# Kernel optimization log

Measured on AMD Instinct MI355X. Metric: run time of the kernel, lower is better.

Reference implementation:

```python
import jax, jax.numpy as jnp
import numpy as np

L, V, Tctx, D, H, DFF = 4, 32000, 1024, 1024, 16, 4096
HD = D // H
B, T = 2, 1024


def _ln(x, w, b):
    mu = jnp.mean(x, axis=-1, keepdims=True)
    var = jnp.var(x, axis=-1, keepdims=True)
    return (x - mu) * jax.lax.rsqrt(var + 1e-5) * w + b


def setup_inputs() -> dict:
    key = jax.random.key(0)
    ks = jax.random.split(key, 8)
    s = 0.02
    return {
        "idx": jax.random.randint(ks[0], (B, T), 0, V),
        "wte": jax.random.normal(ks[1], (V, D), jnp.float32) * s,
        "wpe": jax.random.normal(ks[2], (Tctx, D), jnp.float32) * s,
        "ln1_w": jnp.ones((L, D), jnp.float32),
        "ln1_b": jnp.zeros((L, D), jnp.float32),
        "qkv_w": jax.random.normal(ks[3], (L, 3 * D, D), jnp.float32) * s,
        "qkv_b": jnp.zeros((L, 3 * D), jnp.float32),
        "proj_w": jax.random.normal(ks[4], (L, D, D), jnp.float32) * s,
        "proj_b": jnp.zeros((L, D), jnp.float32),
        "ln2_w": jnp.ones((L, D), jnp.float32),
        "ln2_b": jnp.zeros((L, D), jnp.float32),
        "fc1_w": jax.random.normal(ks[5], (L, DFF, D), jnp.float32) * s,
        "fc1_b": jnp.zeros((L, DFF), jnp.float32),
        "fc2_w": jax.random.normal(ks[6], (L, D, DFF), jnp.float32) * s,
        "fc2_b": jnp.zeros((L, D), jnp.float32),
        "lnf_w": jnp.ones((D,), jnp.float32),
        "lnf_b": jnp.zeros((D,), jnp.float32),
    }


def reference(idx, wte, wpe, ln1_w, ln1_b, qkv_w, qkv_b, proj_w, proj_b,
              ln2_w, ln2_b, fc1_w, fc1_b, fc2_w, fc2_b, lnf_w, lnf_b):
    b, t = idx.shape
    x = wte[idx] + wpe[:t]  # (B,T,D); dropout=0 (eval)
    scale = 1.0 / jnp.sqrt(jnp.float32(HD))
    causal = jnp.tril(jnp.ones((t, t), bool))  # (T,T)

    def block(x, p):
        (l1w, l1b, qw, qb, pw, pb, l2w, l2b, f1w, f1b, f2w, f2b) = p
        h = _ln(x, l1w, l1b)
        qkv = h @ qw.T + qb  # (B,T,3D)
        q, k, v = jnp.split(qkv, 3, axis=-1)
        q = q.reshape(b, t, H, HD)
        k = k.reshape(b, t, H, HD)
        v = v.reshape(b, t, H, HD)
        att = jnp.einsum('bqhd,bkhd->bhqk', q, k) * scale
        att = jnp.where(causal, att, -jnp.inf)
        att = jax.nn.softmax(att, axis=-1)
        y = jnp.einsum('bhqk,bkhd->bqhd', att, v).reshape(b, t, D)
        x = x + y @ pw.T + pb
        h2 = _ln(x, l2w, l2b)
        h2 = jax.nn.gelu(h2 @ f1w.T + f1b, approximate=False)
        x = x + h2 @ f2w.T + f2b
        return x, None

    params = (ln1_w, ln1_b, qkv_w, qkv_b, proj_w, proj_b,
              ln2_w, ln2_b, fc1_w, fc1_b, fc2_w, fc2_b)
    x, _ = jax.lax.scan(block, x, params)
    x = _ln(x, lnf_w, lnf_b)
    logits = x @ wte.T  # weight-tied lm_head
    return logits
```

## Files before the change

kernel.cpp:

```cpp
#include <hip/hip_runtime.h>
#include <hip/hip_bf16.h>
#include <cstdint>
#include <cstddef>

using hb = __hip_bfloat16;
typedef __bf16 bf16x8 __attribute__((ext_vector_type(8)));
typedef float f32x4 __attribute__((ext_vector_type(4)));
typedef const __attribute__((address_space(1))) void* gptr_t;
typedef __attribute__((address_space(3))) void* lptr_t;

namespace {
constexpr int L_ = 4, V_ = 32000, D_ = 1024, H_ = 16, DFF_ = 4096, HD_ = 64;
constexpr int B_ = 2, T_ = 1024;
constexpr int BT = B_ * T_;
constexpr int PSTR = 56;
constexpr int MTILES = BT / 128;
}

__global__ __launch_bounds__(256) void k_cast_bf16(const float* __restrict__ in,
                                                   hb* __restrict__ out, int n4) {
  int i = blockIdx.x * 256 + threadIdx.x;
  const int stride = gridDim.x * 256;
  for (; i < n4; i += stride) {
    float4 v = reinterpret_cast<const float4*>(in)[i];
    union { hb h[4]; ushort4 u; } t;
    t.h[0] = __float2bfloat16(v.x);
    t.h[1] = __float2bfloat16(v.y);
    t.h[2] = __float2bfloat16(v.z);
    t.h[3] = __float2bfloat16(v.w);
    reinterpret_cast<ushort4*>(out)[i] = t.u;
  }
}

__global__ __launch_bounds__(256) void k_embed(const int* __restrict__ idx,
                                               const float* __restrict__ wte,
                                               const float* __restrict__ wpe,
                                               float* __restrict__ x) {
  const int i = blockIdx.x * 256 + threadIdx.x;
  const int row = i >> 10;
  const int d = i & 1023;
  const int t = row & (T_ - 1);
  const int tok = idx[row];
  x[i] = wte[(size_t)tok * D_ + d] + wpe[(size_t)t * D_ + d];
}

__global__ __launch_bounds__(256) void k_ln(const float* __restrict__ x,
                                            const float* __restrict__ w,
                                            const float* __restrict__ b,
                                            hb* __restrict__ out) {
  const int row = blockIdx.x;
  const int tid = threadIdx.x;
  const float4 v = reinterpret_cast<const float4*>(x + (size_t)row * D_)[tid];
  float s = v.x + v.y + v.z + v.w;
  float ss = v.x * v.x + v.y * v.y + v.z * v.z + v.w * v.w;
#pragma unroll
  for (int o = 32; o; o >>= 1) { s += __shfl_xor(s, o); ss += __shfl_xor(ss, o); }
  __shared__ float rs[4], rss[4];
  const int wid = tid >> 6;
  if ((tid & 63) == 0) { rs[wid] = s; rss[wid] = ss; }
  __syncthreads();
  s = rs[0] + rs[1] + rs[2] + rs[3];
  ss = rss[0] + rss[1] + rss[2] + rss[3];
  const float mu = s * (1.f / D_);
  const float var = ss * (1.f / D_) - mu * mu;
  const float rstd = rsqrtf(var + 1e-5f);
  const float4 wv = reinterpret_cast<const float4*>(w)[tid];
  const float4 bv = reinterpret_cast<const float4*>(b)[tid];
  union { hb h[4]; ushort4 u; } t;
  t.h[0] = __float2bfloat16((v.x - mu) * rstd * wv.x + bv.x);
  t.h[1] = __float2bfloat16((v.y - mu) * rstd * wv.y + bv.y);
  t.h[2] = __float2bfloat16((v.z - mu) * rstd * wv.z + bv.z);
  t.h[3] = __float2bfloat16((v.w - mu) * rstd * wv.w + bv.w);
  reinterpret_cast<ushort4*>(out + (size_t)row * D_)[tid] = t.u;
}

__global__ __launch_bounds__(256) void k_vtrans(const hb* __restrict__ qkv,
                                                hb* __restrict__ vt) {
  __shared__ __align__(16) hb tile[64][66];
  const int bh = blockIdx.x;
  const int b = bh >> 4, h = bh & (H_ - 1);
  const int t0 = blockIdx.y * 64;
  const int tid = threadIdx.x;
  const int tl = tid >> 2, dc = (tid & 3) * 16;
  const hb* src = qkv + ((size_t)(b * T_ + t0 + tl) * 3 * D_) + 2 * D_ + h * HD_ + dc;
  *reinterpret_cast<bf16x8*>(&tile[tl][dc]) = *reinterpret_cast<const bf16x8*>(src);
  *reinterpret_cast<bf16x8*>(&tile[tl][dc + 8]) = *reinterpret_cast<const bf16x8*>(src + 8);
  __syncthreads();
  const int d = tid & 63, tj = tid >> 6;
  hb o[16];
#pragma unroll
  for (int j = 0; j < 16; ++j) o[j] = tile[tj * 16 + j][d];
  bf16x8* dst = reinterpret_cast<bf16x8*>(vt + ((size_t)bh * HD_ + d) * T_ + t0 + tj * 16);
  dst[0] = *reinterpret_cast<bf16x8*>(&o[0]);
  dst[1] = *reinterpret_cast<bf16x8*>(&o[8]);
}

__global__ __launch_bounds__(256) void k_attn(const hb* __restrict__ qkv,
                                              const hb* __restrict__ vt,
                                              hb* __restrict__ y) {
  const int lane = threadIdx.x & 63;
  const int wid = threadIdx.x >> 6;
  const int gw = blockIdx.x * 4 + wid;
  const int qt = 63 - (gw & 63);
  const int bh = gw >> 6;
  const int h = bh & (H_ - 1), b = bh >> 4;
  const int q0 = qt * 16;
  const int lr = lane & 15, g = lane >> 4;

  __shared__ __align__(16) hb plds[4][16 * PSTR];
  hb* pw = plds[wid];

  const size_t qrow = ((size_t)(b * T_ + q0 + lr) * 3 * D_) + (size_t)h * HD_;
  const bf16x8 qa0 = *reinterpret_cast<const bf16x8*>(qkv + qrow + g * 8);
  const bf16x8 qa1 = *reinterpret_cast<const bf16x8*>(qkv + qrow + 32 + g * 8);

  const f32x4 z = {0.f, 0.f, 0.f, 0.f};
  float m[4] = {-1e30f, -1e30f, -1e30f, -1e30f};
  float lsum[4] = {0.f, 0.f, 0.f, 0.f};
  f32x4 o[4];
#pragma unroll
  for (int i = 0; i < 4; ++i) o[i] = z;

  const int nkv = (q0 + 47) >> 5;
  for (int kt = 0; kt < nkv; ++kt) {
    const int kv0 = kt * 32;
    f32x4 s[2];
#pragma unroll
    for (int nt = 0; nt < 2; ++nt) {
      const size_t krow =
          ((size_t)(b * T_ + kv0 + nt * 16 + lr) * 3 * D_) + D_ + (size_t)h * HD_;
      const bf16x8 kb0 = *reinterpret_cast<const bf16x8*>(qkv + krow + g * 8);
      const bf16x8 kb1 = *reinterpret_cast<const bf16x8*>(qkv + krow + 32 + g * 8);
      f32x4 acc = z;
      acc = __builtin_amdgcn_mfma_f32_16x16x32_bf16(qa0, kb0, acc, 0, 0, 0);
      acc = __builtin_amdgcn_mfma_f32_16x16x32_bf16(qa1, kb1, acc, 0, 0, 0);
      s[nt] = acc;
    }
#pragma unroll
    for (int r = 0; r < 4; ++r) {
      const int qg = q0 + g * 4 + r;
      const float s0 = (kv0 + lr <= qg) ? s[0][r] * 0.125f : -1e30f;
      const float s1 = (kv0 + 16 + lr <= qg) ? s[1][r] * 0.125f : -1e30f;
      float rmax = fmaxf(s0, s1);
#pragma unroll
      for (int off = 1; off < 16; off <<= 1) rmax = fmaxf(rmax, __shfl_xor(rmax, off));
      const float mn = fmaxf(m[r], rmax);
      const float c = __expf(m[r] - mn);
      m[r] = mn;
      const float p0 = __expf(s0 - mn);
      const float p1 = __expf(s1 - mn);
      float ps = p0 + p1;
#pragma unroll
      for (int off = 1; off < 16; off <<= 1) ps += __shfl_xor(ps, off);
      lsum[r] = lsum[r] * c + ps;
#pragma unroll
      for (int dt = 0; dt < 4; ++dt) o[dt][r] *= c;
      pw[(g * 4 + r) * PSTR + lr] = __float2bfloat16(p0);
      pw[(g * 4 + r) * PSTR + 16 + lr] = __float2bfloat16(p1);
    }
    const bf16x8 pa = *reinterpret_cast<const bf16x8*>(&pw[lr * PSTR + g * 8]);
#pragma unroll
    for (int dt = 0; dt < 4; ++dt) {
      const bf16x8 vb = *reinterpret_cast<const bf16x8*>(
          vt + ((size_t)bh * HD_ + dt * 16 + lr) * T_ + kv0 + g * 8);
      o[dt] = __builtin_amdgcn_mfma_f32_16x16x32_bf16(pa, vb, o[dt], 0, 0, 0);
    }
  }
#pragma unroll
  for (int dt = 0; dt < 4; ++dt) {
#pragma unroll
    for (int r = 0; r < 4; ++r) {
      const size_t oo =
          ((size_t)(b * T_ + q0 + g * 4 + r) * D_) + h * HD_ + dt * 16 + lr;
      y[oo] = __float2bfloat16(o[dt][r] / lsum[r]);
    }
  }
}

template <int EPI, bool OBF, int BN>
__global__ __launch_bounds__(256) void gemm_bt(const hb* __restrict__ A,
                                               const hb* __restrict__ Bw,
                                               const float* __restrict__ bias,
                                               const float* resid,
                                               void* outv, int M, int N, int K) {
  constexpr int WMR = (BN == 128) ? 4 : 2;
  __shared__ __align__(16) hb As[2][128 * 32];
  __shared__ __align__(16) hb Bs[2][BN * 32];
  const int tid = threadIdx.x, lane = tid & 63, wid = tid >> 6;

  const int nwg = gridDim.x;
  const int d = blockIdx.x;
  const int wg = (d & 7) * (nwg >> 3) + (d >> 3);
  const int m0 = (wg & (MTILES - 1)) * 128;
  const int n0 = (wg / MTILES) * BN;

  const int wr = (BN == 128) ? (wid >> 1) : wid;
  const int wc = (BN == 128) ? (wid & 1) : 0;

  f32x4 acc[WMR][4];
  const f32x4 z = {0.f, 0.f, 0.f, 0.f};
#pragma unroll
  for (int i = 0; i < WMR; ++i)
#pragma unroll
    for (int j = 0; j < 4; ++j) acc[i][j] = z;

  const int e0 = tid * 8;
  auto stage = [&](int buf, int k0) {
#pragma unroll
    for (int r = 0; r < 2; ++r) {
      const int e = e0 + r * 2048;
      const int row = e >> 5, col = e & 31;
      __builtin_amdgcn_global_load_lds(
          (gptr_t)(A + (size_t)(m0 + row) * K + k0 + col), (lptr_t)(&As[buf][e]), 16, 0, 0);
    }
#pragma unroll
    for (int r = 0; r < BN / 64; ++r) {
      const int e = e0 + r * 2048;
      const int row = e >> 5, col = e & 31;
      __builtin_amdgcn_global_load_lds(
          (gptr_t)(Bw + (size_t)(n0 + row) * K + k0 + col), (lptr_t)(&Bs[buf][e]), 16, 0, 0);
    }
  };

  stage(0, 0);
  stage(1, 32);

  const int nt = K >> 5;
  const int lr = lane & 15, lk = (lane >> 4) * 8;
  for (int t = 0; t < nt; ++t) {
    const int cur = t & 1;
    if (t + 1 < nt) {
      if constexpr (BN == 128)
        asm volatile("s_waitcnt vmcnt(4)" ::: "memory");
      else
        asm volatile("s_waitcnt vmcnt(3)" ::: "memory");
    } else {
      asm volatile("s_waitcnt vmcnt(0)" ::: "memory");
    }
    asm volatile("s_barrier" ::: "memory");

    bf16x8 af[WMR], bfr[4];
#pragma unroll
    for (int i = 0; i < WMR; ++i)
      af[i] = *reinterpret_cast<const bf16x8*>(
          &As[cur][(wr * (WMR * 16) + i * 16 + lr) * 32 + lk]);
#pragma unroll
    for (int j = 0; j < 4; ++j)
      bfr[j] = *reinterpret_cast<const bf16x8*>(
          &Bs[cur][(wc * 64 + j * 16 + lr) * 32 + lk]);
#pragma unroll
    for (int i = 0; i < WMR; ++i)
#pragma unroll
      for (int j = 0; j < 4; ++j)
        acc[i][j] = __builtin_amdgcn_mfma_f32_16x16x32_bf16(af[i], bfr[j], acc[i][j], 0, 0, 0);

    asm volatile("s_waitcnt lgkmcnt(0)" ::: "memory");
    asm volatile("s_barrier" ::: "memory");
    if (t + 2 < nt) stage(cur, (t + 2) * 32);
  }

  const int lc = lane & 15, lr4 = (lane >> 4) * 4;
#pragma unroll
  for (int i = 0; i < WMR; ++i) {
    const int grow0 = m0 + wr * (WMR * 16) + i * 16 + lr4;
#pragma unroll
    for (int j = 0; j < 4; ++j) {
      const int gcol = n0 + wc * 64 + j * 16 + lc;
      const float bv = bias ? bias[gcol] : 0.f;
#pragma unroll
      for (int r = 0; r < 4; ++r) {
        const size_t oo = (size_t)(grow0 + r) * N + gcol;
        float val = acc[i][j][r] + bv;
        if constexpr (EPI == 1) val += resid[oo];
        if constexpr (EPI == 2) val = 0.5f * val * (1.f + erff(val * 0.70710678118f));
        if constexpr (OBF)
          reinterpret_cast<hb*>(outv)[oo] = __float2bfloat16(val);
        else
          reinterpret_cast<float*>(outv)[oo] = val;
      }
    }
  }
}

extern "C" void kernel_launch(void* const* d_in, const int* in_sizes, int n_in,
                              void* d_out, int out_size, void* d_ws, size_t ws_size,
                              hipStream_t stream) {
  const int* idx = (const int*)d_in[0];
  const float* wte = (const float*)d_in[1];
  const float* wpe = (const float*)d_in[2];
  const float* ln1_w = (const float*)d_in[3];
  const float* ln1_b = (const float*)d_in[4];
  const float* qkv_w = (const float*)d_in[5];
  const float* qkv_b = (const float*)d_in[6];
  const float* proj_w = (const float*)d_in[7];
  const float* proj_b = (const float*)d_in[8];
  const float* ln2_w = (const float*)d_in[9];
  const float* ln2_b = (const float*)d_in[10];
  const float* fc1_w = (const float*)d_in[11];
  const float* fc1_b = (const float*)d_in[12];
  const float* fc2_w = (const float*)d_in[13];
  const float* fc2_b = (const float*)d_in[14];
  const float* lnf_w = (const float*)d_in[15];
  const float* lnf_b = (const float*)d_in[16];

  char* ws = (char*)d_ws;
  size_t off = 0;
  auto alloc = [&](size_t bytes) -> void* {
    void* p = ws + off;
    off += (bytes + 255) & ~(size_t)255;
    return p;
  };
  hb* wte_bf = (hb*)alloc((size_t)V_ * D_ * 2);
  hb* qkvw_bf = (hb*)alloc((size_t)L_ * 3 * D_ * D_ * 2);
  hb* projw_bf = (hb*)alloc((size_t)L_ * D_ * D_ * 2);
  hb* fc1w_bf = (hb*)alloc((size_t)L_ * DFF_ * D_ * 2);
  hb* fc2w_bf = (hb*)alloc((size_t)L_ * D_ * DFF_ * 2);
  float* x = (float*)alloc((size_t)BT * D_ * 4);
  hb* hbuf = (hb*)alloc((size_t)BT * D_ * 2);
  hb* qkvbuf = (hb*)alloc((size_t)BT * 3 * D_ * 2);
  hb* ybuf = (hb*)alloc((size_t)BT * D_ * 2);
  hb* gbuf = (hb*)alloc((size_t)BT * DFF_ * 2);
  hb* vtbuf = (hb*)alloc((size_t)B_ * H_ * HD_ * T_ * 2);

  auto cast = [&](const float* src, hb* dst, size_t n) {
    int n4 = (int)(n / 4);
    int blocks = (n4 + 255) / 256;
    if (blocks > 4096) blocks = 4096;
    k_cast_bf16<<<blocks, 256, 0, stream>>>(src, dst, n4);
  };
  cast(wte, wte_bf, (size_t)V_ * D_);
  cast(qkv_w, qkvw_bf, (size_t)L_ * 3 * D_ * D_);
  cast(proj_w, projw_bf, (size_t)L_ * D_ * D_);
  cast(fc1_w, fc1w_bf, (size_t)L_ * DFF_ * D_);
  cast(fc2_w, fc2w_bf, (size_t)L_ * D_ * DFF_);

  k_embed<<<BT * D_ / 256, 256, 0, stream>>>(idx, wte, wpe, x);

  for (int l = 0; l < L_; ++l) {
    k_ln<<<BT, 256, 0, stream>>>(x, ln1_w + l * D_, ln1_b + l * D_, hbuf);
    gemm_bt<0, true, 128><<<MTILES * (3 * D_ / 128), 256, 0, stream>>>(
        hbuf, qkvw_bf + (size_t)l * 3 * D_ * D_, qkv_b + (size_t)l * 3 * D_, nullptr,
        qkvbuf, BT, 3 * D_, D_);
    k_vtrans<<<dim3(B_ * H_, T_ / 64), 256, 0, stream>>>(qkvbuf, vtbuf);
    k_attn<<<(B_ * H_ * (T_ / 16)) / 4, 256, 0, stream>>>(qkvbuf, vtbuf, ybuf);
    gemm_bt<1, false, 64><<<MTILES * (D_ / 64), 256, 0, stream>>>(
        ybuf, projw_bf + (size_t)l * D_ * D_, proj_b + (size_t)l * D_, x, x, BT, D_, D_);
    k_ln<<<BT, 256, 0, stream>>>(x, ln2_w + l * D_, ln2_b + l * D_, hbuf);
    gemm_bt<2, true, 128><<<MTILES * (DFF_ / 128), 256, 0, stream>>>(
        hbuf, fc1w_bf + (size_t)l * DFF_ * D_, fc1_b + (size_t)l * DFF_, nullptr,
        gbuf, BT, DFF_, D_);
    gemm_bt<1, false, 64><<<MTILES * (D_ / 64), 256, 0, stream>>>(
        gbuf, fc2w_bf + (size_t)l * D_ * DFF_, fc2_b + (size_t)l * D_, x, x, BT, D_, DFF_);
  }

  k_ln<<<BT, 256, 0, stream>>>(x, lnf_w, lnf_b, hbuf);
  gemm_bt<0, false, 128><<<MTILES * (V_ / 128), 256, 0, stream>>>(
      hbuf, wte_bf, nullptr, nullptr, d_out, BT, V_, D_);
}
```

Baseline: 1.255 ms.

## Add dedicated 256x256 pipelined LM-head GEMM kernel with direct-to-LDS loads

Replaces the generic 128-tile GEMM for the weight-tied LM head with a specialized kernel: 512 threads, 256x256 output tiles, double-buffered LDS filled via global_load_lds, swizzled LDS layout, interleaved MFMA and staging with setprio, and an XCD-aware block remap. It targets the largest GEMM (2048x32000x1024) and aims for better operand reuse and overlap of loads with MFMA. Large register footprint (128 accumulators) and hardcoded shapes that rely on 32000 being divisible by 256 are the trade-offs.

```diff
diff --git a/kernel.cpp b/kernel.cpp
--- a/kernel.cpp
+++ b/kernel.cpp
@@ -278,6 +278,130 @@
         else
           reinterpret_cast<float*>(outv)[oo] = val;
       }
+    }
+  }
+}
+
+#define MM16(ABASE, AF, BF)                                                     \
+  _Pragma("unroll") for (int i_ = 0; i_ < 4; ++i_)                              \
+      _Pragma("unroll") for (int j_ = 0; j_ < 4; ++j_)                          \
+          acc[(ABASE) + i_][j_] = __builtin_amdgcn_mfma_f32_16x16x32_bf16(      \
+              (AF)[i_], (BF)[j_], acc[(ABASE) + i_][j_], 0, 0, 0);
+
+__global__ __launch_bounds__(512, 2) void gemm_lmhead(const hb* __restrict__ A,
+                                                      const hb* __restrict__ Bw,
+                                                      float* __restrict__ out) {
+  constexpr int K = 1024, N = 32000, NTK = K / 64;
+  __shared__ __align__(16) hb As[2][2][256][32];
+  __shared__ __align__(16) hb Bs[2][2][256][32];
+  const int tid = threadIdx.x, lane = tid & 63, wid = tid >> 6;
+  const int nwg = gridDim.x;
+  const int dd = blockIdx.x;
+  const int wg = (dd & 7) * (nwg >> 3) + (dd >> 3);
+  const int m0 = (wg & 7) * 256;
+  const int n0 = (wg >> 3) * 256;
+  const int wr = wid >> 2, wc = wid & 3;
+  const int lr = lane & 15;
+  const int rc8 = (((lane >> 4) ^ ((lr >> 1) & 3)) & 3) * 8;
+
+  f32x4 acc[8][4];
+  const f32x4 z = {0.f, 0.f, 0.f, 0.f};
+#pragma unroll
+  for (int i = 0; i < 8; ++i)
+#pragma unroll
+    for (int j = 0; j < 4; ++j) acc[i][j] = z;
+
+  const int rr = tid >> 2;
+  const int cs = tid & 3;
+  const int cc = cs ^ ((tid >> 3) & 3);
+
+  auto stageA = [&](int b, int kk, int kt) {
+#pragma unroll
+    for (int q = 0; q < 2; ++q) {
+      const int row = q * 128 + rr;
+      __builtin_amdgcn_global_load_lds(
+          (gptr_t)(A + (size_t)(m0 + row) * K + kt * 64 + kk * 32 + cc * 8),
+          (lptr_t)(&As[b][kk][row][cs * 8]), 16, 0, 0);
+    }
+  };
+  auto stageB = [&](int b, int kk, int kt) {
+#pragma unroll
+    for (int q = 0; q < 2; ++q) {
+      const int row = q * 128 + rr;
+      __builtin_amdgcn_global_load_lds(
+          (gptr_t)(Bw + (size_t)(n0 + row) * K + kt * 64 + kk * 32 + cc * 8),
+          (lptr_t)(&Bs[b][kk][row][cs * 8]), 16, 0, 0);
+    }
+  };
+  auto dsA = [&](int b, int kk, int mh, bf16x8* af) {
+#pragma unroll
+    for (int i = 0; i < 4; ++i)
+      af[i] = *reinterpret_cast<const bf16x8*>(
+          &As[b][kk][wr * 128 + mh * 64 + i * 16 + lr][rc8]);
+  };
+  auto dsB = [&](int b, int kk, bf16x8* bf) {
+#pragma unroll
+    for (int j = 0; j < 4; ++j)
+      bf[j] = *reinterpret_cast<const bf16x8*>(&Bs[b][kk][wc * 64 + j * 16 + lr][rc8]);
+  };
+
+  auto ktile = [&](int c, int kt, bool st, bool last) {
+    bf16x8 af[4], bf[4];
+    asm volatile("s_waitcnt vmcnt(4)" ::: "memory");
+    __builtin_amdgcn_s_barrier();
+    dsA(c, 0, 0, af);
+    dsB(c, 0, bf);
+    if (st) { stageA(c ^ 1, 0, kt + 1); stageB(c ^ 1, 0, kt + 1); }
+    __builtin_amdgcn_s_setprio(1);
+    MM16(0, af, bf)
+    __builtin_amdgcn_s_setprio(0);
+    __builtin_amdgcn_s_barrier();
+    dsA(c, 0, 1, af);
+    if (st) { stageA(c ^ 1, 1, kt + 1); stageB(c ^ 1, 1, kt + 1); }
+    __builtin_amdgcn_s_setprio(1);
+    MM16(4, af, bf)
+    __builtin_amdgcn_s_setprio(0);
+    __builtin_amdgcn_s_barrier();
+    if (last)
+      asm volatile("s_waitcnt vmcnt(0)" ::: "memory");
+    else
+      asm volatile("s_waitcnt vmcnt(8)" ::: "memory");
+    __builtin_amdgcn_s_barrier();
+    dsA(c, 1, 0, af);
+    dsB(c, 1, bf);
+    __builtin_amdgcn_s_setprio(1);
+    MM16(0, af, bf)
+    __builtin_amdgcn_s_setprio(0);
+    __builtin_amdgcn_s_barrier();
+    dsA(c, 1, 1, af);
+    __builtin_amdgcn_s_setprio(1);
+    MM16(4, af, bf)
+    __builtin_amdgcn_s_setprio(0);
+    __builtin_amdgcn_s_barrier();
+  };
+
+  stageA(0, 0, 0);
+  stageB(0, 0, 0);
+  stageA(0, 1, 0);
+  stageB(0, 1, 0);
+
+  for (int t = 0; t < NTK - 2; t += 2) {
+    ktile(0, t, true, false);
+    ktile(1, t + 1, true, false);
+  }
+  ktile(0, NTK - 2, true, false);
+  ktile(1, NTK - 1, false, true);
+
+  const int lc = lane & 15, lr4 = (lane >> 4) * 4;
+#pragma unroll
+  for (int i2 = 0; i2 < 8; ++i2) {
+    const int grow0 = m0 + wr * 128 + i2 * 16 + lr4;
+#pragma unroll
+    for (int j = 0; j < 4; ++j) {
+      const int gcol = n0 + wc * 64 + j * 16 + lc;
+#pragma unroll
+      for (int r = 0; r < 4; ++r)
+        out[(size_t)(grow0 + r) * N + gcol] = acc[i2][j][r];
     }
   }
 }
@@ -354,6 +478,5 @@
   }
 
   k_ln<<<BT, 256, 0, stream>>>(x, lnf_w, lnf_b, hbuf);
-  gemm_bt<0, false, 128><<<MTILES * (V_ / 128), 256, 0, stream>>>(
-      hbuf, wte_bf, nullptr, nullptr, d_out, BT, V_, D_);
-}
+  gemm_lmhead<<<8 * (V_ / 256), 512, 0, stream>>>(hbuf, wte_bf, (float*)d_out);
+}
```

New measurement: 1.228 ms. 1.02x faster.
